# Optimization experiments

Hardware: AMD Instinct MI355X
Metric: run time of the kernel (lower is better)

The kernel has to match this reference:

```python
import jax, jax.numpy as jnp
import numpy as np

B, T, D, U = 32, 2048, 512, 512

def setup_inputs() -> dict:
    key = jax.random.key(0)
    ks = jax.random.split(key, 8)
    s = 0.02
    return {
        "query": jax.random.normal(ks[0], (B, D), dtype=jnp.float32),
        "values": jax.random.normal(ks[1], (B, T, D), dtype=jnp.float32),
        "W1_w": jax.random.normal(ks[2], (D, U), dtype=jnp.float32) * s,
        "W1_b": jnp.zeros((U,), dtype=jnp.float32),
        "W2_w": jax.random.normal(ks[3], (D, U), dtype=jnp.float32) * s,
        "W2_b": jnp.zeros((U,), dtype=jnp.float32),
        "V_w": jax.random.normal(ks[4], (U, 1), dtype=jnp.float32) * s,
        "V_b": jnp.zeros((1,), dtype=jnp.float32),
    }

def reference(query, values, W1_w, W1_b, W2_w, W2_b, V_w, V_b):
    # query: [B, D] -> [B, 1, U]; values: [B, T, D] -> [B, T, U]
    q_proj = (query @ W1_w + W1_b)[:, None, :]              # [B, 1, U]
    v_proj = jnp.einsum('btd,du->btu', values, W2_w) + W2_b  # [B, T, U]
    score = jnp.tanh(q_proj + v_proj) @ V_w + V_b            # [B, T, 1]
    attn = jax.nn.softmax(score, axis=1)                     # [B, T, 1]
    context = jnp.sum(attn * values, axis=1)                 # [B, D]
    return context, attn
```

## Files before the change

kernel.cpp:

```cpp
#include <hip/hip_runtime.h>
#include <hip/hip_bf16.h>
#include <cstddef>
#include <cstdint>

#define B_ 32
#define T_ 2048
#define D_ 512
#define U_ 512

typedef __attribute__((ext_vector_type(8))) short bf16x8;
typedef __attribute__((ext_vector_type(4))) float f32x4;

__device__ __forceinline__ unsigned short f2bf(float f) {
  union { float f; unsigned u; } x; x.f = f;
  unsigned r = x.u + 0x7fffu + ((x.u >> 16) & 1u);
  return (unsigned short)(r >> 16);
}
__device__ __forceinline__ float tanh_fast(float x) {
  float e = __expf(2.0f * x);
  return 1.0f - 2.0f * __builtin_amdgcn_rcpf(e + 1.0f);
}

#define AS1C(p) ((const __attribute__((address_space(1))) unsigned*)(p))
#define AS3(p)  ((__attribute__((address_space(3))) unsigned*)(p))

__global__ void kA_prep(const float* __restrict__ W2, unsigned* __restrict__ W2P,
                        const float* __restrict__ query, const float* __restrict__ W1,
                        const float* __restrict__ W1b, const float* __restrict__ W2b,
                        float* __restrict__ qp, float* __restrict__ score,
                        float* __restrict__ ctx) {
  const int tid = threadIdx.x;
  if (blockIdx.x < 16) {
    const int kg = blockIdx.x;
    __shared__ unsigned short w2s[32][514];
    const float4* W2v = (const float4*)(W2 + (size_t)kg * 32 * U_);
    #pragma unroll
    for (int i = 0; i < 16; ++i) {
      int idx = i * 256 + tid;
      float4 v = W2v[idx];
      int r = idx >> 7, c = (idx & 127) * 4;
      w2s[r][c + 0] = f2bf(v.x); w2s[r][c + 1] = f2bf(v.y);
      w2s[r][c + 2] = f2bf(v.z); w2s[r][c + 3] = f2bf(v.w);
    }
    __syncthreads();
    const int lq = tid >> 6, lr = (tid >> 2) & 15, j = tid & 3;
    const int kb = lq * 8 + j * 2;
    #pragma unroll
    for (int ut = 0; ut < 32; ++ut)
      W2P[ut * 4096 + kg * 256 + tid] =
          (unsigned)w2s[kb][ut * 16 + lr] | ((unsigned)w2s[kb + 1][ut * 16 + lr] << 16);
  } else {
    __shared__ float qs[D_];
    const int blk = blockIdx.x - 16;
    const int b = blk >> 1, uhh = (blk & 1) * 256;
    qs[tid] = query[b * D_ + tid];
    qs[tid + 256] = query[b * D_ + tid + 256];
    __syncthreads();
    const int u = uhh + tid;
    float a0 = 0, a1 = 0, a2 = 0, a3 = 0, a4 = 0, a5 = 0, a6 = 0, a7 = 0;
    for (int d = 0; d < D_; d += 8) {
      a0 += qs[d + 0] * W1[(size_t)(d + 0) * U_ + u];
      a1 += qs[d + 1] * W1[(size_t)(d + 1) * U_ + u];
      a2 += qs[d + 2] * W1[(size_t)(d + 2) * U_ + u];
      a3 += qs[d + 3] * W1[(size_t)(d + 3) * U_ + u];
      a4 += qs[d + 4] * W1[(size_t)(d + 4) * U_ + u];
      a5 += qs[d + 5] * W1[(size_t)(d + 5) * U_ + u];
      a6 += qs[d + 6] * W1[(size_t)(d + 6) * U_ + u];
      a7 += qs[d + 7] * W1[(size_t)(d + 7) * U_ + u];
    }
    qp[b * U_ + u] = ((a0 + a1) + (a2 + a3)) + ((a4 + a5) + (a6 + a7)) + W1b[u] + W2b[u];
    const int gt = blk * 256 + tid;
    ctx[gt] = 0.0f;
    #pragma unroll
    for (int i = 0; i < 4; ++i) score[i * 16384 + gt] = 0.0f;
  }
}

__global__ __launch_bounds__(256, 2) void k2_dma(
    const float* __restrict__ values, const unsigned short* __restrict__ W2P,
    const float* __restrict__ qp, const float* __restrict__ Vw,
    float* __restrict__ score) {
  __shared__ float av[4][4096];
  const int tid = threadIdx.x;
  const int bx = blockIdx.x;
  const int mt = bx >> 1, uh = bx & 1;
  const int m0 = mt * 64;
  const int b = m0 >> 11;
  const int l = tid & 63, w = tid >> 6;
  const int lr = l & 15, lq = l >> 4;

  const int drow = l >> 4;
  const int dchunk = l & 15;

  f32x4 acc[4][4];
  #pragma unroll
  for (int mi = 0; mi < 4; ++mi)
    #pragma unroll
    for (int ni = 0; ni < 4; ++ni) acc[mi][ni] = (f32x4){0.f, 0.f, 0.f, 0.f};

  const unsigned short* Bb = W2P + (size_t)(uh * 16 + w * 4) * 8192 + (size_t)l * 8;

  auto stage = [&](int s) {
    const int p = s & 3;
    #pragma unroll
    for (int j = 0; j < 4; ++j) {
      int g = w * 4 + j;
      int row = g * 4 + drow;
      int q = dchunk ^ (row & 15);
      const float* gp = values + (size_t)(m0 + row) * D_ + s * 64 + q * 4;
      __builtin_amdgcn_global_load_lds(AS1C(gp), AS3(&av[p][g * 256]), 16, 0, 0);
    }
  };

  bf16x8 Bf[2][8];
  auto loadB = [&](int ph) {
    const int slot = ph & 1;
    #pragma unroll
    for (int kq = 0; kq < 2; ++kq)
      #pragma unroll
      for (int ni = 0; ni < 4; ++ni)
        Bf[slot][kq * 4 + ni] =
            *(const bf16x8*)(Bb + (size_t)ni * 8192 + (size_t)(2 * ph + kq) * 512);
  };

  loadB(0);
  stage(0);
  loadB(1);
  stage(1);

  #pragma unroll
  for (int e = 0; e < 8; ++e) {
    __builtin_amdgcn_sched_barrier(0);
    if (e == 7) asm volatile("s_waitcnt vmcnt(8)" ::: "memory");
    else        asm volatile("s_waitcnt vmcnt(12)" ::: "memory");
    __builtin_amdgcn_s_barrier();
    __builtin_amdgcn_sched_barrier(0);
    if (e < 7) loadB(e + 1);
    if (e < 6) stage(e + 2);

    #pragma unroll
    for (int kq = 0; kq < 2; ++kq) {
      bf16x8 a[4];
      #pragma unroll
      for (int mi = 0; mi < 4; ++mi) {
        const int row = mi * 16 + lr;
        const int p0 = (kq * 8 + lq * 2) ^ lr;
        f32x4 flo = *(const f32x4*)&av[e & 3][row * 64 + (p0 << 2)];
        f32x4 fhi = *(const f32x4*)&av[e & 3][row * 64 + ((p0 ^ 1) << 2)];
        union { bf16x8 v; __hip_bfloat162 h[4]; } A;
        A.h[0] = __float22bfloat162_rn(make_float2(flo.x, flo.y));
        A.h[1] = __float22bfloat162_rn(make_float2(flo.z, flo.w));
        A.h[2] = __float22bfloat162_rn(make_float2(fhi.x, fhi.y));
        A.h[3] = __float22bfloat162_rn(make_float2(fhi.z, fhi.w));
        a[mi] = A.v;
      }
      __builtin_amdgcn_s_setprio(1);
      #pragma unroll
      for (int ni = 0; ni < 4; ++ni)
        #pragma unroll
        for (int mi = 0; mi < 4; ++mi)
          acc[mi][ni] = __builtin_amdgcn_mfma_f32_16x16x32_bf16(
              a[mi], Bf[e & 1][kq * 4 + ni], acc[mi][ni], 0, 0, 0);
      __builtin_amdgcn_s_setprio(0);
    }
  }

  float sacc[4][4];
  #pragma unroll
  for (int mi = 0; mi < 4; ++mi)
    #pragma unroll
    for (int r = 0; r < 4; ++r) sacc[mi][r] = 0.0f;
  #pragma unroll
  for (int ni = 0; ni < 4; ++ni) {
    int u = uh * 256 + w * 64 + ni * 16 + lr;
    float qpv = qp[b * U_ + u], vv = Vw[u];
    #pragma unroll
    for (int mi = 0; mi < 4; ++mi)
      #pragma unroll
      for (int r = 0; r < 4; ++r)
        sacc[mi][r] += tanh_fast(acc[mi][ni][r] + qpv) * vv;
  }
  #pragma unroll
  for (int mi = 0; mi < 4; ++mi)
    #pragma unroll
    for (int r = 0; r < 4; ++r) {
      float v = sacc[mi][r];
      v += __shfl_xor(v, 1); v += __shfl_xor(v, 2);
      v += __shfl_xor(v, 4); v += __shfl_xor(v, 8);
      if (lr == 0) atomicAdd(&score[m0 + mi * 16 + lq * 4 + r], v);
    }
}

__global__ void k3_softmax(const float* __restrict__ score, float* __restrict__ attn) {
  __shared__ float red[8];
  const int b = blockIdx.x, tid = threadIdx.x;
  const float* s = score + b * T_;
  float v[8];
  float mx = -1e30f;
  #pragma unroll
  for (int i = 0; i < 8; ++i) { v[i] = s[tid + i * 256]; mx = fmaxf(mx, v[i]); }
  #pragma unroll
  for (int off = 1; off < 64; off <<= 1) mx = fmaxf(mx, __shfl_xor(mx, off));
  if ((tid & 63) == 0) red[tid >> 6] = mx;
  __syncthreads();
  mx = fmaxf(fmaxf(red[0], red[1]), fmaxf(red[2], red[3]));
  float sum = 0.0f;
  #pragma unroll
  for (int i = 0; i < 8; ++i) { v[i] = __expf(v[i] - mx); sum += v[i]; }
  #pragma unroll
  for (int off = 1; off < 64; off <<= 1) sum += __shfl_xor(sum, off);
  if ((tid & 63) == 0) red[4 + (tid >> 6)] = sum;
  __syncthreads();
  sum = (red[4] + red[5]) + (red[6] + red[7]);
  float inv = 1.0f / sum;
  #pragma unroll
  for (int i = 0; i < 8; ++i) attn[b * T_ + tid + i * 256] = v[i] * inv;
}

__global__ void k4_ctx(const float* __restrict__ values, const float* __restrict__ attn,
                       float* __restrict__ ctx) {
  __shared__ float at[64];
  __shared__ float ps[512];
  const int blk = blockIdx.x;
  const int b = blk >> 5, tc = blk & 31;
  const int tid = threadIdx.x;
  if (tid < 64) at[tid] = attn[b * T_ + tc * 64 + tid];
  __syncthreads();
  const int q = tid & 127;
  const int r0 = tid >> 7;
  const float4* vb = (const float4*)(values + ((size_t)b * T_ + tc * 64) * D_);
  float ax = 0.f, ay = 0.f, az = 0.f, aw = 0.f;
  #pragma unroll 8
  for (int tt = 0; tt < 32; ++tt) {
    int row = tt * 2 + r0;
    float4 v = vb[(size_t)row * 128 + q];
    float a = at[row];
    ax += a * v.x; ay += a * v.y; az += a * v.z; aw += a * v.w;
  }
  if (r0 == 1) { ps[4 * q] = ax; ps[4 * q + 1] = ay; ps[4 * q + 2] = az; ps[4 * q + 3] = aw; }
  __syncthreads();
  if (r0 == 0) {
    atomicAdd(&ctx[b * D_ + 4 * q + 0], ax + ps[4 * q + 0]);
    atomicAdd(&ctx[b * D_ + 4 * q + 1], ay + ps[4 * q + 1]);
    atomicAdd(&ctx[b * D_ + 4 * q + 2], az + ps[4 * q + 2]);
    atomicAdd(&ctx[b * D_ + 4 * q + 3], aw + ps[4 * q + 3]);
  }
}

extern "C" void kernel_launch(void* const* d_in, const int* in_sizes, int n_in,
                              void* d_out, int out_size, void* d_ws, size_t ws_size,
                              hipStream_t stream) {
  const float* query = (const float*)d_in[0];
  const float* values = (const float*)d_in[1];
  const float* W1w = (const float*)d_in[2];
  const float* W1b = (const float*)d_in[3];
  const float* W2w = (const float*)d_in[4];
  const float* W2b = (const float*)d_in[5];
  const float* Vw  = (const float*)d_in[6];

  float* out = (float*)d_out;
  float* ctx  = out;
  float* attn = out + B_ * D_;
  float* score = attn;

  char* ws = (char*)d_ws;
  unsigned* W2P = (unsigned*)ws;
  float* qp    = (float*)(ws + 512 * 1024);

  kA_prep<<<80, 256, 0, stream>>>(W2w, W2P, query, W1w, W1b, W2b, qp, score, ctx);
  k2_dma<<<2048, 256, 0, stream>>>(values, (const unsigned short*)W2P, qp, Vw, score);
  k3_softmax<<<32, 256, 0, stream>>>(score, attn);
  k4_ctx<<<1024, 256, 0, stream>>>(values, attn, ctx);
}
```

Before: 279.2 us.

## Fuse score, unnormalized softmax and context into one pass over values

The scoring GEMM kernel now covers all 512 units per 32-row tile, so each block holds the full score and no atomics on score are needed. Scores are exponentiated against a fixed bound C = sum|Vw|, which removes the softmax max pass. Each block then computes its unnormalized context contribution from values while the tile is still hot in cache. A small final kernel normalizes attn and scales ctx, so the separate ctx pass and its second full read of values are gone. In exchange, values are converted to bf16 through registers into LDS instead of using async global-to-LDS DMA, and W2P B-fragments are read from global on every k-step. Subtracting C instead of the true max risks underflow for large |Vw| sums.

```diff
diff --git a/kernel.cpp b/kernel.cpp
--- a/kernel.cpp
+++ b/kernel.cpp
@@ -21,14 +21,22 @@
   return 1.0f - 2.0f * __builtin_amdgcn_rcpf(e + 1.0f);
 }
 
-#define AS1C(p) ((const __attribute__((address_space(1))) unsigned*)(p))
-#define AS3(p)  ((__attribute__((address_space(3))) unsigned*)(p))
+__device__ __forceinline__ void wave0_sumabs_vw(const float* __restrict__ Vw,
+                                                float* Cs, int tid) {
+  if (tid < 64) {
+    float c = 0.f;
+    #pragma unroll
+    for (int i = 0; i < 8; ++i) c += fabsf(Vw[tid + i * 64]);
+    c += __shfl_xor(c, 1);  c += __shfl_xor(c, 2);  c += __shfl_xor(c, 4);
+    c += __shfl_xor(c, 8);  c += __shfl_xor(c, 16); c += __shfl_xor(c, 32);
+    if (tid == 0) *Cs = c;
+  }
+}
 
 __global__ void kA_prep(const float* __restrict__ W2, unsigned* __restrict__ W2P,
                         const float* __restrict__ query, const float* __restrict__ W1,
                         const float* __restrict__ W1b, const float* __restrict__ W2b,
-                        float* __restrict__ qp, float* __restrict__ score,
-                        float* __restrict__ ctx) {
+                        float* __restrict__ qp, float* __restrict__ ctx) {
   const int tid = threadIdx.x;
   if (blockIdx.x < 16) {
     const int kg = blockIdx.x;
@@ -71,180 +79,157 @@
     qp[b * U_ + u] = ((a0 + a1) + (a2 + a3)) + ((a4 + a5) + (a6 + a7)) + W1b[u] + W2b[u];
     const int gt = blk * 256 + tid;
     ctx[gt] = 0.0f;
-    #pragma unroll
-    for (int i = 0; i < 4; ++i) score[i * 16384 + gt] = 0.0f;
-  }
-}
-
-__global__ __launch_bounds__(256, 2) void k2_dma(
+  }
+}
+
+__global__ __launch_bounds__(512, 4) void k2attn(
     const float* __restrict__ values, const unsigned short* __restrict__ W2P,
     const float* __restrict__ qp, const float* __restrict__ Vw,
-    float* __restrict__ score) {
-  __shared__ float av[4][4096];
+    float* __restrict__ score, float* __restrict__ ctxU) {
+  __shared__ __align__(16) float avb[4][1024];
+  __shared__ float sred[8][32];
+  __shared__ float ps2[32];
+  __shared__ float Cs;
+
   const int tid = threadIdx.x;
   const int bx = blockIdx.x;
-  const int mt = bx >> 1, uh = bx & 1;
-  const int m0 = mt * 64;
+  const int m0 = bx * 32;
   const int b = m0 >> 11;
   const int l = tid & 63, w = tid >> 6;
   const int lr = l & 15, lq = l >> 4;
 
-  const int drow = l >> 4;
-  const int dchunk = l & 15;
-
-  f32x4 acc[4][4];
-  #pragma unroll
-  for (int mi = 0; mi < 4; ++mi)
+  const int row_st = w * 4 + (l >> 4);
+  const int fseg = l & 15;
+  const float* vrow = values + (size_t)(m0 + row_st) * D_ + fseg * 4;
+
+  f32x4 acc[2][4];
+  #pragma unroll
+  for (int mi = 0; mi < 2; ++mi)
     #pragma unroll
     for (int ni = 0; ni < 4; ++ni) acc[mi][ni] = (f32x4){0.f, 0.f, 0.f, 0.f};
 
-  const unsigned short* Bb = W2P + (size_t)(uh * 16 + w * 4) * 8192 + (size_t)l * 8;
-
-  auto stage = [&](int s) {
-    const int p = s & 3;
-    #pragma unroll
-    for (int j = 0; j < 4; ++j) {
-      int g = w * 4 + j;
-      int row = g * 4 + drow;
-      int q = dchunk ^ (row & 15);
-      const float* gp = values + (size_t)(m0 + row) * D_ + s * 64 + q * 4;
-      __builtin_amdgcn_global_load_lds(AS1C(gp), AS3(&av[p][g * 256]), 16, 0, 0);
-    }
+  const unsigned short* Bb = W2P + (size_t)(w * 4) * 8192 + (size_t)l * 8;
+
+  auto consume = [&](float4 g, int s) {
+    __hip_bfloat162 h0 = __float22bfloat162_rn(make_float2(g.x, g.y));
+    __hip_bfloat162 h1 = __float22bfloat162_rn(make_float2(g.z, g.w));
+    union { __hip_bfloat162 h; unsigned u; } c0, c1; c0.h = h0; c1.h = h1;
+    int slot = (fseg >> 1) ^ (row_st & 7);
+    char* dst = (char*)avb[s & 3] + row_st * 128 + (slot << 4) + ((fseg & 1) << 3);
+    *(uint2*)dst = make_uint2(c0.u, c1.u);
   };
 
-  bf16x8 Bf[2][8];
-  auto loadB = [&](int ph) {
-    const int slot = ph & 1;
-    #pragma unroll
-    for (int kq = 0; kq < 2; ++kq)
-      #pragma unroll
-      for (int ni = 0; ni < 4; ++ni)
-        Bf[slot][kq * 4 + ni] =
-            *(const bf16x8*)(Bb + (size_t)ni * 8192 + (size_t)(2 * ph + kq) * 512);
-  };
-
-  loadB(0);
-  stage(0);
-  loadB(1);
-  stage(1);
+  wave0_sumabs_vw(Vw, &Cs, tid);
+
+  float4 Ga = *(const float4*)(vrow);
+  float4 Gb = *(const float4*)(vrow + 64);
+  float4 Gc = *(const float4*)(vrow + 128);
+  consume(Ga, 0);
+  consume(Gb, 1);
+  __syncthreads();
+  const float C = Cs;
+  float4 Gcons = Gc;
 
   #pragma unroll
   for (int e = 0; e < 8; ++e) {
+    float4 Gnew = (float4){0.f, 0.f, 0.f, 0.f};
+    if (e < 5) Gnew = *(const float4*)(vrow + (e + 3) * 64);
+    const char* buf = (const char*)avb[e & 3];
+    #pragma unroll
+    for (int kq = 0; kq < 2; ++kq) {
+      const int kg = e * 2 + kq;
+      const int sl = ((kq << 2) | lq) ^ (lr & 7);
+      bf16x8 a0 = *(const bf16x8*)(buf + (lr) * 128 + (sl << 4));
+      bf16x8 a1 = *(const bf16x8*)(buf + (16 + lr) * 128 + (sl << 4));
+      bf16x8 b0 = *(const bf16x8*)(Bb + 0 * 8192 + (size_t)kg * 512);
+      bf16x8 b1 = *(const bf16x8*)(Bb + 1 * 8192 + (size_t)kg * 512);
+      bf16x8 b2 = *(const bf16x8*)(Bb + 2 * 8192 + (size_t)kg * 512);
+      bf16x8 b3 = *(const bf16x8*)(Bb + 3 * 8192 + (size_t)kg * 512);
+      __builtin_amdgcn_s_setprio(1);
+      acc[0][0] = __builtin_amdgcn_mfma_f32_16x16x32_bf16(a0, b0, acc[0][0], 0, 0, 0);
+      acc[1][0] = __builtin_amdgcn_mfma_f32_16x16x32_bf16(a1, b0, acc[1][0], 0, 0, 0);
+      acc[0][1] = __builtin_amdgcn_mfma_f32_16x16x32_bf16(a0, b1, acc[0][1], 0, 0, 0);
+      acc[1][1] = __builtin_amdgcn_mfma_f32_16x16x32_bf16(a1, b1, acc[1][1], 0, 0, 0);
+      acc[0][2] = __builtin_amdgcn_mfma_f32_16x16x32_bf16(a0, b2, acc[0][2], 0, 0, 0);
+      acc[1][2] = __builtin_amdgcn_mfma_f32_16x16x32_bf16(a1, b2, acc[1][2], 0, 0, 0);
+      acc[0][3] = __builtin_amdgcn_mfma_f32_16x16x32_bf16(a0, b3, acc[0][3], 0, 0, 0);
+      acc[1][3] = __builtin_amdgcn_mfma_f32_16x16x32_bf16(a1, b3, acc[1][3], 0, 0, 0);
+      __builtin_amdgcn_s_setprio(0);
+      if (kq == 0 && e < 6) consume(Gcons, e + 2);
+    }
+    Gcons = Gnew;
     __builtin_amdgcn_sched_barrier(0);
-    if (e == 7) asm volatile("s_waitcnt vmcnt(8)" ::: "memory");
-    else        asm volatile("s_waitcnt vmcnt(12)" ::: "memory");
+    asm volatile("s_waitcnt lgkmcnt(0)" ::: "memory");
     __builtin_amdgcn_s_barrier();
     __builtin_amdgcn_sched_barrier(0);
-    if (e < 7) loadB(e + 1);
-    if (e < 6) stage(e + 2);
-
-    #pragma unroll
-    for (int kq = 0; kq < 2; ++kq) {
-      bf16x8 a[4];
-      #pragma unroll
-      for (int mi = 0; mi < 4; ++mi) {
-        const int row = mi * 16 + lr;
-        const int p0 = (kq * 8 + lq * 2) ^ lr;
-        f32x4 flo = *(const f32x4*)&av[e & 3][row * 64 + (p0 << 2)];
-        f32x4 fhi = *(const f32x4*)&av[e & 3][row * 64 + ((p0 ^ 1) << 2)];
-        union { bf16x8 v; __hip_bfloat162 h[4]; } A;
-        A.h[0] = __float22bfloat162_rn(make_float2(flo.x, flo.y));
-        A.h[1] = __float22bfloat162_rn(make_float2(flo.z, flo.w));
-        A.h[2] = __float22bfloat162_rn(make_float2(fhi.x, fhi.y));
-        A.h[3] = __float22bfloat162_rn(make_float2(fhi.z, fhi.w));
-        a[mi] = A.v;
-      }
-      __builtin_amdgcn_s_setprio(1);
-      #pragma unroll
-      for (int ni = 0; ni < 4; ++ni)
-        #pragma unroll
-        for (int mi = 0; mi < 4; ++mi)
-          acc[mi][ni] = __builtin_amdgcn_mfma_f32_16x16x32_bf16(
-              a[mi], Bf[e & 1][kq * 4 + ni], acc[mi][ni], 0, 0, 0);
-      __builtin_amdgcn_s_setprio(0);
-    }
-  }
-
-  float sacc[4][4];
-  #pragma unroll
-  for (int mi = 0; mi < 4; ++mi)
+  }
+
+  float sacc[2][4];
+  #pragma unroll
+  for (int mi = 0; mi < 2; ++mi)
     #pragma unroll
     for (int r = 0; r < 4; ++r) sacc[mi][r] = 0.0f;
   #pragma unroll
   for (int ni = 0; ni < 4; ++ni) {
-    int u = uh * 256 + w * 64 + ni * 16 + lr;
+    int u = (w * 4 + ni) * 16 + lr;
     float qpv = qp[b * U_ + u], vv = Vw[u];
     #pragma unroll
-    for (int mi = 0; mi < 4; ++mi)
+    for (int mi = 0; mi < 2; ++mi)
       #pragma unroll
       for (int r = 0; r < 4; ++r)
         sacc[mi][r] += tanh_fast(acc[mi][ni][r] + qpv) * vv;
   }
   #pragma unroll
-  for (int mi = 0; mi < 4; ++mi)
+  for (int mi = 0; mi < 2; ++mi)
     #pragma unroll
     for (int r = 0; r < 4; ++r) {
       float v = sacc[mi][r];
       v += __shfl_xor(v, 1); v += __shfl_xor(v, 2);
       v += __shfl_xor(v, 4); v += __shfl_xor(v, 8);
-      if (lr == 0) atomicAdd(&score[m0 + mi * 16 + lq * 4 + r], v);
-    }
-}
-
-__global__ void k3_softmax(const float* __restrict__ score, float* __restrict__ attn) {
-  __shared__ float red[8];
+      if (lr == 0) sred[w][mi * 16 + lq * 4 + r] = v;
+    }
+  __syncthreads();
+
+  if (tid < 32) {
+    float s = 0.f;
+    #pragma unroll
+    for (int wv = 0; wv < 8; ++wv) s += sred[wv][tid];
+    score[m0 + tid] = s;
+    ps2[tid] = __expf(s - C);
+  }
+  __syncthreads();
+
+  float accc = 0.f;
+  const int col = tid;
+  #pragma unroll 4
+  for (int row = 0; row < 32; ++row)
+    accc += ps2[row] * values[(size_t)(m0 + row) * D_ + col];
+  atomicAdd(&ctxU[(size_t)b * D_ + col], accc);
+}
+
+__global__ void kB_final(const float* __restrict__ Vw, float* __restrict__ attn,
+                         float* __restrict__ ctx) {
+  __shared__ float Cs;
+  __shared__ float red[4];
   const int b = blockIdx.x, tid = threadIdx.x;
-  const float* s = score + b * T_;
-  float v[8];
-  float mx = -1e30f;
-  #pragma unroll
-  for (int i = 0; i < 8; ++i) { v[i] = s[tid + i * 256]; mx = fmaxf(mx, v[i]); }
-  #pragma unroll
-  for (int off = 1; off < 64; off <<= 1) mx = fmaxf(mx, __shfl_xor(mx, off));
-  if ((tid & 63) == 0) red[tid >> 6] = mx;
-  __syncthreads();
-  mx = fmaxf(fmaxf(red[0], red[1]), fmaxf(red[2], red[3]));
-  float sum = 0.0f;
-  #pragma unroll
-  for (int i = 0; i < 8; ++i) { v[i] = __expf(v[i] - mx); sum += v[i]; }
+  wave0_sumabs_vw(Vw, &Cs, tid);
+  __syncthreads();
+  const float C = Cs;
+  float* s = attn + b * T_;
+  float p[8];
+  float sum = 0.f;
+  #pragma unroll
+  for (int i = 0; i < 8; ++i) { p[i] = __expf(s[tid + i * 256] - C); sum += p[i]; }
   #pragma unroll
   for (int off = 1; off < 64; off <<= 1) sum += __shfl_xor(sum, off);
-  if ((tid & 63) == 0) red[4 + (tid >> 6)] = sum;
-  __syncthreads();
-  sum = (red[4] + red[5]) + (red[6] + red[7]);
-  float inv = 1.0f / sum;
-  #pragma unroll
-  for (int i = 0; i < 8; ++i) attn[b * T_ + tid + i * 256] = v[i] * inv;
-}
-
-__global__ void k4_ctx(const float* __restrict__ values, const float* __restrict__ attn,
-                       float* __restrict__ ctx) {
-  __shared__ float at[64];
-  __shared__ float ps[512];
-  const int blk = blockIdx.x;
-  const int b = blk >> 5, tc = blk & 31;
-  const int tid = threadIdx.x;
-  if (tid < 64) at[tid] = attn[b * T_ + tc * 64 + tid];
-  __syncthreads();
-  const int q = tid & 127;
-  const int r0 = tid >> 7;
-  const float4* vb = (const float4*)(values + ((size_t)b * T_ + tc * 64) * D_);
-  float ax = 0.f, ay = 0.f, az = 0.f, aw = 0.f;
-  #pragma unroll 8
-  for (int tt = 0; tt < 32; ++tt) {
-    int row = tt * 2 + r0;
-    float4 v = vb[(size_t)row * 128 + q];
-    float a = at[row];
-    ax += a * v.x; ay += a * v.y; az += a * v.z; aw += a * v.w;
-  }
-  if (r0 == 1) { ps[4 * q] = ax; ps[4 * q + 1] = ay; ps[4 * q + 2] = az; ps[4 * q + 3] = aw; }
-  __syncthreads();
-  if (r0 == 0) {
-    atomicAdd(&ctx[b * D_ + 4 * q + 0], ax + ps[4 * q + 0]);
-    atomicAdd(&ctx[b * D_ + 4 * q + 1], ay + ps[4 * q + 1]);
-    atomicAdd(&ctx[b * D_ + 4 * q + 2], az + ps[4 * q + 2]);
-    atomicAdd(&ctx[b * D_ + 4 * q + 3], aw + ps[4 * q + 3]);
-  }
+  if ((tid & 63) == 0) red[tid >> 6] = sum;
+  __syncthreads();
+  sum = (red[0] + red[1]) + (red[2] + red[3]);
+  const float inv = 1.0f / sum;
+  #pragma unroll
+  for (int i = 0; i < 8; ++i) attn[b * T_ + tid + i * 256] = p[i] * inv;
+  #pragma unroll
+  for (int i = 0; i < 2; ++i) ctx[b * D_ + tid + i * 256] *= inv;
 }
 
 extern "C" void kernel_launch(void* const* d_in, const int* in_sizes, int n_in,
@@ -267,8 +252,7 @@
   unsigned* W2P = (unsigned*)ws;
   float* qp    = (float*)(ws + 512 * 1024);
 
-  kA_prep<<<80, 256, 0, stream>>>(W2w, W2P, query, W1w, W1b, W2b, qp, score, ctx);
-  k2_dma<<<2048, 256, 0, stream>>>(values, (const unsigned short*)W2P, qp, Vw, score);
-  k3_softmax<<<32, 256, 0, stream>>>(score, attn);
-  k4_ctx<<<1024, 256, 0, stream>>>(values, attn, ctx);
-}
+  kA_prep<<<80, 256, 0, stream>>>(W2w, W2P, query, W1w, W1b, W2b, qp, ctx);
+  k2attn<<<2048, 512, 0, stream>>>(values, (const unsigned short*)W2P, qp, Vw, score, ctx);
+  kB_final<<<32, 256, 0, stream>>>(Vw, attn, ctx);
+}
```

Result: no change. 274.9 us (-1.5%).
